# Performance work log

Measured on AMD Instinct MI355X. Metric: run time of the kernel, lower is better.

Reference implementation:

```python
import jax, jax.numpy as jnp
import numpy as np
import math

B, HW, E = 128, 3136, 96
NH, WS = 3, 7
EH = E // NH
NEG_INF = float('-inf')


def setup_inputs() -> dict:
    key = jax.random.key(0)
    ks = jax.random.split(key, 5)
    x = jax.random.normal(ks[0], (B, HW, E), dtype=jnp.float32)
    w1 = jax.random.normal(ks[1], (3 * E, E), dtype=jnp.float32) * 0.02
    b1 = jnp.zeros((3 * E,), dtype=jnp.float32)
    w2 = jax.random.normal(ks[2], (E, E), dtype=jnp.float32) * 0.02
    b2 = jnp.zeros((E,), dtype=jnp.float32)
    return {"x": x, "w1": w1, "b1": b1, "w2": w2, "b2": b2}


def _masks():
    m = WS * (WS // 2)  # 21
    row = jnp.zeros((WS * WS, WS * WS), dtype=jnp.float32)
    row = row.at[-m:, :-m].set(NEG_INF)
    row = row.at[:-m, -m:].set(NEG_INF)
    # rearrange '(r w1) (c w2) -> (w1 r) (w2 c)'
    col = row.reshape(WS, WS, WS, WS).transpose(1, 0, 3, 2).reshape(WS * WS, WS * WS)
    return row, col


def reference(x, w1, b1, w2, b2):
    b = x.shape[0]
    hh = ww = int(round(math.sqrt(x.shape[1])))
    nh, nw = hh // WS, ww // WS
    qkv = x @ w1.T + b1                      # [b, hw, 3E]
    qkv = qkv.reshape(b, hh, ww, E, 3)       # (c K) split, K=3
    # cyclic shift: (-WS)//2 == -4 (faithful to torch source)
    s = (-WS) // 2
    qkv = jnp.roll(qkv, (s, s), axis=(1, 2))
    # window partition: b (h m1) (w m2) (H E) K -> b H h w (m1 m2) E K
    t = qkv.reshape(b, nh, WS, nw, WS, NH, EH, 3)
    t = t.transpose(0, 5, 1, 3, 2, 4, 6, 7).reshape(b, NH, nh, nw, WS * WS, EH, 3)
    q, k, v = t[..., 0], t[..., 1], t[..., 2]
    att = jnp.einsum('bHxyqe,bHxyke->bHxyqk', q, k) / math.sqrt(EH)
    row_mask, col_mask = _masks()
    att = att.at[:, :, -1, :].add(row_mask)
    att = att.at[:, :, :, -1].add(col_mask)
    p = jax.nn.softmax(att, axis=-1)
    o = jnp.einsum('bHxyqk,bHxyke->bHxyqe', p, v)
    # reverse window partition: b H h w (m1 m2) E -> b (h m1) (w m2) (H E)
    o = o.reshape(b, NH, nh, nw, WS, WS, EH)
    o = o.transpose(0, 2, 4, 3, 5, 1, 6).reshape(b, hh, ww, E)
    o = jnp.roll(o, (WS // 2, WS // 2), axis=(1, 2))  # +3 (faithful)
    o = o.reshape(b, hh * ww, E)
    return o @ w2.T + b2
```

## Files before the change

### kernel.cpp

```cpp
#include <hip/hip_runtime.h>

typedef __attribute__((ext_vector_type(8))) __bf16 bf16x8;
typedef __attribute__((ext_vector_type(4))) float f32x4;
typedef __attribute__((ext_vector_type(4))) unsigned int u32x4;

__device__ __forceinline__ unsigned short f2bf(float f){
    unsigned int x = __builtin_bit_cast(unsigned int, f);
    x += 0x7FFFu + ((x >> 16) & 1u);
    return (unsigned short)(x >> 16);
}
__device__ __forceinline__ unsigned int pk2(float a, float b){
    return (unsigned int)f2bf(a) | ((unsigned int)f2bf(b) << 16);
}
__device__ __forceinline__ bf16x8 ldfrag(const unsigned short* p){
    u32x4 v = *reinterpret_cast<const u32x4*>(p);
    return __builtin_bit_cast(bf16x8, v);
}
__device__ __forceinline__ bf16x8 ldf32(const float* p){
    f32x4 a = *reinterpret_cast<const f32x4*>(p);
    f32x4 b = *reinterpret_cast<const f32x4*>(p + 4);
    u32x4 r;
    r[0] = pk2(a[0], a[1]); r[1] = pk2(a[2], a[3]);
    r[2] = pk2(b[0], b[1]); r[3] = pk2(b[2], b[3]);
    return __builtin_bit_cast(bf16x8, r);
}
__device__ __forceinline__ f32x4 mfma_bf16(bf16x8 a, bf16x8 b, f32x4 c){
    return __builtin_amdgcn_mfma_f32_16x16x32_bf16(a, b, c, 0, 0, 0);
}

#define W1F_SH 27648
#define W2F_SH 9216

__global__ __launch_bounds__(256) void k_prep(const float* __restrict__ w1,
                                              const float* __restrict__ b1,
                                              const float* __restrict__ w2,
                                              unsigned short* __restrict__ w1f,
                                              unsigned short* __restrict__ w2f,
                                              float* __restrict__ b1p)
{
    const float SCALE = 0.17677669529663687f;
    int i = blockIdx.x * 256 + threadIdx.x;
    if (i < 3456){
        int f = i >> 6, lane = i & 63;
        int n = f / 3, ks = f - n * 3;
        int l15 = lane & 15, qd = lane >> 4;
        int rp = n * 16 + l15;
        int c = rp / 96, rem = rp - c * 96;
        float s = (c == 0) ? SCALE : 1.0f;
        const float* src = w1 + (size_t)(3 * rem + c) * 96 + ks * 32 + qd * 8;
        f32x4 v0 = *reinterpret_cast<const f32x4*>(src);
        f32x4 v1 = *reinterpret_cast<const f32x4*>(src + 4);
        u32x4 p;
        p[0] = pk2(v0[0] * s, v0[1] * s); p[1] = pk2(v0[2] * s, v0[3] * s);
        p[2] = pk2(v1[0] * s, v1[1] * s); p[3] = pk2(v1[2] * s, v1[3] * s);
        *reinterpret_cast<u32x4*>(w1f + (size_t)f * 512 + lane * 8) = p;
    } else if (i < 4608){
        int j = i - 3456;
        int f = j >> 6, lane = j & 63;
        int n = f / 3, ks = f - n * 3;
        int l15 = lane & 15, qd = lane >> 4;
        const float* src = w2 + (size_t)(n * 16 + l15) * 96 + ks * 32 + qd * 8;
        f32x4 v0 = *reinterpret_cast<const f32x4*>(src);
        f32x4 v1 = *reinterpret_cast<const f32x4*>(src + 4);
        u32x4 p;
        p[0] = pk2(v0[0], v0[1]); p[1] = pk2(v0[2], v0[3]);
        p[2] = pk2(v1[0], v1[1]); p[3] = pk2(v1[2], v1[3]);
        *reinterpret_cast<u32x4*>(w2f + (size_t)f * 512 + lane * 8) = p;
    } else if (i < 4896){
        int rp = i - 4608;
        int c = rp / 96, rem = rp - c * 96;
        b1p[rp] = b1[3 * rem + c] * ((c == 0) ? SCALE : 1.0f);
    }
}

__global__ __launch_bounds__(256, 5) void k_fused(const float* __restrict__ x,
                                                  const unsigned short* __restrict__ w1f,
                                                  const float* __restrict__ b1p,
                                                  const unsigned short* __restrict__ w2f,
                                                  const float* __restrict__ b2,
                                                  float* __restrict__ out)
{
    __shared__ __align__(16) unsigned short smem[13056];
    unsigned short* Kr = smem;
    unsigned short* Vt = smem + 6144;
    float* o2 = reinterpret_cast<float*>(smem);

    const int tid = threadIdx.x;
    const int win = blockIdx.x;
    const int b = win >> 6, wy = (win >> 3) & 7, wx = win & 7;
    const int wave = tid >> 6, lane = tid & 63;
    const int l15 = lane & 15, qd = lane >> 4;
    const int s0 = (qd & 1) * 32 + l15;
    const int s1 = s0 + 16;

    bf16x8 bQf[3];
    {
        int pos = wave * 16 + l15;
        int iy = pos / 7, ix = pos - iy * 7;
        int h = wy * 7 + iy + 4; if (h >= 56) h -= 56;
        int w = wx * 7 + ix + 4; if (w >= 56) w -= 56;
        const float* xr = x + ((size_t)b * 3136 + h * 56 + w) * 96;
        bf16x8 aX0 = ldf32(xr + qd * 8);
        bf16x8 aX1 = ldf32(xr + 32 + qd * 8);
        bf16x8 aX2 = ldf32(xr + 64 + qd * 8);

        unsigned int Qw[12];
#pragma unroll
        for (int qt = 0; qt < 6; ++qt){
            const unsigned short* wf = w1f + (size_t)(qt * 3) * 512 + lane * 8;
            f32x4 a = {0.f, 0.f, 0.f, 0.f};
            a = mfma_bf16(ldfrag(wf),        aX0, a);
            a = mfma_bf16(ldfrag(wf + 512),  aX1, a);
            a = mfma_bf16(ldfrag(wf + 1024), aX2, a);
            f32x4 bq = *reinterpret_cast<const f32x4*>(b1p + qt * 16 + qd * 4);
            Qw[qt * 2]     = pk2(a[0] + bq[0], a[1] + bq[1]);
            Qw[qt * 2 + 1] = pk2(a[2] + bq[2], a[3] + bq[3]);
        }
#pragma unroll
        for (int H = 0; H < 3; ++H){
            u32x4 qw; unsigned int lo, hi;
            lo = (unsigned)__shfl((int)Qw[(2*H)*2],     s0, 64);
            hi = (unsigned)__shfl((int)Qw[(2*H+1)*2],   s0, 64); qw[0] = (qd & 2) ? hi : lo;
            lo = (unsigned)__shfl((int)Qw[(2*H)*2+1],   s0, 64);
            hi = (unsigned)__shfl((int)Qw[(2*H+1)*2+1], s0, 64); qw[1] = (qd & 2) ? hi : lo;
            lo = (unsigned)__shfl((int)Qw[(2*H)*2],     s1, 64);
            hi = (unsigned)__shfl((int)Qw[(2*H+1)*2],   s1, 64); qw[2] = (qd & 2) ? hi : lo;
            lo = (unsigned)__shfl((int)Qw[(2*H)*2+1],   s1, 64);
            hi = (unsigned)__shfl((int)Qw[(2*H+1)*2+1], s1, 64); qw[3] = (qd & 2) ? hi : lo;
            bQf[H] = __builtin_bit_cast(bf16x8, qw);
        }

#pragma unroll
        for (int n = 0; n < 6; ++n){
            const unsigned short* wf = w1f + (size_t)((6 + n) * 3) * 512 + lane * 8;
            f32x4 a = {0.f, 0.f, 0.f, 0.f};
            a = mfma_bf16(aX0, ldfrag(wf),        a);
            a = mfma_bf16(aX1, ldfrag(wf + 512),  a);
            a = mfma_bf16(aX2, ldfrag(wf + 1024), a);
            float bb = b1p[(6 + n) * 16 + l15];
            int H = n >> 1;
            int eh = ((n & 1) << 4) + l15;
            int ch = eh >> 3;
#pragma unroll
            for (int r = 0; r < 4; ++r){
                int p = wave * 16 + qd * 4 + r;
                int chs = ch ^ ((p >> 1) & 3);
                Kr[H * 2048 + p * 32 + chs * 8 + (eh & 7)] = f2bf(a[r] + bb);
            }
        }
#pragma unroll
        for (int n = 0; n < 6; ++n){
            const unsigned short* wf = w1f + (size_t)((12 + n) * 3) * 512 + lane * 8;
            f32x4 a = {0.f, 0.f, 0.f, 0.f};
            a = mfma_bf16(aX0, ldfrag(wf),        a);
            a = mfma_bf16(aX1, ldfrag(wf + 512),  a);
            a = mfma_bf16(aX2, ldfrag(wf + 1024), a);
            float bb = b1p[(12 + n) * 16 + l15];
            int H = n >> 1;
            int eh = ((n & 1) << 4) + l15;
#pragma unroll
            for (int r = 0; r < 4; ++r){
                int p = wave * 16 + qd * 4 + r;
                Vt[(H * 32 + eh) * 72 + p] = f2bf(a[r] + bb);
            }
        }
    }
    __syncthreads();

    const bool rowm = (wy == 7), colm = (wx == 7);
    const float NEGINF = -__builtin_inff();
    unsigned int m49 = 0, m28 = 0, m7 = 0;
#pragma unroll
    for (int tn = 0; tn < 4; ++tn)
#pragma unroll
        for (int r = 0; r < 4; ++r){
            int col = tn * 16 + qd * 4 + r;
            int bit = tn * 4 + r;
            m49 |= (unsigned)(col >= 49) << bit;
            m28 |= (unsigned)(col >= 28) << bit;
            m7  |= (unsigned)((col % 7) >= 4) << bit;
        }
    const int qrow = wave * 16 + l15;
    const bool rhi = (qrow >= 28);
    const bool rc7 = ((qrow % 7) >= 4);
    const int chq = qd ^ ((l15 >> 1) & 3);

    unsigned int Ow[12];
#pragma unroll
    for (int H = 0; H < 3; ++H){
        f32x4 S[4];
#pragma unroll
        for (int tn = 0; tn < 4; ++tn){
            bf16x8 aK = ldfrag(Kr + H * 2048 + (tn * 16 + l15) * 32 + chq * 8);
            f32x4 z = {0.f, 0.f, 0.f, 0.f};
            S[tn] = mfma_bf16(aK, bQf[H], z);
        }
        float mx = NEGINF;
#pragma unroll
        for (int tn = 0; tn < 4; ++tn)
#pragma unroll
            for (int r = 0; r < 4; ++r){
                int bit = tn * 4 + r;
                float v = S[tn][r];
                bool blocked = (((m49 >> bit) & 1u) != 0u)
                    || (rowm && (rhi != (((m28 >> bit) & 1u) != 0u)))
                    || (colm && (rc7 != (((m7 >> bit) & 1u) != 0u)));
                v = blocked ? NEGINF : v;
                S[tn][r] = v;
                mx = fmaxf(mx, v);
            }
        mx = fmaxf(mx, __shfl_xor(mx, 16, 64));
        mx = fmaxf(mx, __shfl_xor(mx, 32, 64));
        float sum = 0.f;
#pragma unroll
        for (int tn = 0; tn < 4; ++tn)
#pragma unroll
            for (int r = 0; r < 4; ++r){
                float e = exp2f((S[tn][r] - mx) * 1.4426950408889634f);
                S[tn][r] = e;
                sum += e;
            }
        sum += __shfl_xor(sum, 16, 64);
        sum += __shfl_xor(sum, 32, 64);
        float inv = 1.f / sum;

        unsigned int pkv[8];
#pragma unroll
        for (int tn = 0; tn < 4; ++tn){
            pkv[tn * 2]     = pk2(S[tn][0], S[tn][1]);
            pkv[tn * 2 + 1] = pk2(S[tn][2], S[tn][3]);
        }
        bf16x8 pF[2];
#pragma unroll
        for (int kt = 0; kt < 2; ++kt){
            u32x4 aw;
#pragma unroll
            for (int w4 = 0; w4 < 4; ++w4){
                int srcl = (w4 < 2) ? s0 : s1;
                unsigned int lo = (unsigned)__shfl((int)pkv[(2 * kt) * 2 + (w4 & 1)], srcl, 64);
                unsigned int hi = (unsigned)__shfl((int)pkv[(2 * kt + 1) * 2 + (w4 & 1)], srcl, 64);
                aw[w4] = (qd & 2) ? hi : lo;
            }
            pF[kt] = __builtin_bit_cast(bf16x8, aw);
        }
#pragma unroll
        for (int et = 0; et < 2; ++et){
            f32x4 o = {0.f, 0.f, 0.f, 0.f};
#pragma unroll
            for (int kt = 0; kt < 2; ++kt){
                bf16x8 aV = ldfrag(Vt + (H * 32 + et * 16 + l15) * 72 + kt * 32 + qd * 8);
                o = mfma_bf16(aV, pF[kt], o);
            }
            Ow[(H * 2 + et) * 2]     = pk2(o[0] * inv, o[1] * inv);
            Ow[(H * 2 + et) * 2 + 1] = pk2(o[2] * inv, o[3] * inv);
        }
    }

    bf16x8 aO[3];
#pragma unroll
    for (int c = 0; c < 3; ++c){
        u32x4 qw; unsigned int lo, hi;
        lo = (unsigned)__shfl((int)Ow[(2*c)*2],     s0, 64);
        hi = (unsigned)__shfl((int)Ow[(2*c+1)*2],   s0, 64); qw[0] = (qd & 2) ? hi : lo;
        lo = (unsigned)__shfl((int)Ow[(2*c)*2+1],   s0, 64);
        hi = (unsigned)__shfl((int)Ow[(2*c+1)*2+1], s0, 64); qw[1] = (qd & 2) ? hi : lo;
        lo = (unsigned)__shfl((int)Ow[(2*c)*2],     s1, 64);
        hi = (unsigned)__shfl((int)Ow[(2*c+1)*2],   s1, 64); qw[2] = (qd & 2) ? hi : lo;
        lo = (unsigned)__shfl((int)Ow[(2*c)*2+1],   s1, 64);
        hi = (unsigned)__shfl((int)Ow[(2*c+1)*2+1], s1, 64); qw[3] = (qd & 2) ? hi : lo;
        aO[c] = __builtin_bit_cast(bf16x8, qw);
    }

    f32x4 acc2[6];
#pragma unroll
    for (int n = 0; n < 6; ++n){
        const unsigned short* wf = w2f + (size_t)(n * 3) * 512 + lane * 8;
        f32x4 a = {0.f, 0.f, 0.f, 0.f};
        a = mfma_bf16(aO[0], ldfrag(wf),        a);
        a = mfma_bf16(aO[1], ldfrag(wf + 512),  a);
        a = mfma_bf16(aO[2], ldfrag(wf + 1024), a);
        acc2[n] = a;
    }
    __syncthreads();

#pragma unroll
    for (int n = 0; n < 6; ++n){
        float bb = b2[n * 16 + l15];
#pragma unroll
        for (int r = 0; r < 4; ++r)
            o2[(wave * 16 + qd * 4 + r) * 100 + n * 16 + l15] = acc2[n][r] + bb;
    }
    __syncthreads();

    {
        int row = tid >> 2, seg = tid & 3;
        if (row < 49){
            int iy = row / 7, ix = row - iy * 7;
            int h = wy * 7 + iy + 3; if (h >= 56) h -= 56;
            int w = wx * 7 + ix + 3; if (w >= 56) w -= 56;
            const float* src = o2 + row * 100 + seg * 24;
            float* dst = out + ((size_t)b * 3136 + h * 56 + w) * 96 + seg * 24;
#pragma unroll
            for (int v = 0; v < 6; ++v){
                f32x4 t4;
#pragma unroll
                for (int j = 0; j < 4; ++j) t4[j] = src[v * 4 + j];
                *reinterpret_cast<f32x4*>(dst + v * 4) = t4;
            }
        }
    }
}

extern "C" void kernel_launch(void* const* d_in, const int* in_sizes, int n_in,
                              void* d_out, int out_size, void* d_ws, size_t ws_size,
                              hipStream_t stream)
{
    const float* x  = (const float*)d_in[0];
    const float* w1 = (const float*)d_in[1];
    const float* b1 = (const float*)d_in[2];
    const float* w2 = (const float*)d_in[3];
    const float* b2 = (const float*)d_in[4];
    float* out = (float*)d_out;

    unsigned short* w1f = (unsigned short*)d_ws;
    unsigned short* w2f = w1f + W1F_SH;
    float* b1p = (float*)(w2f + W2F_SH);

    hipLaunchKernelGGL(k_prep,  dim3(20),   dim3(256), 0, stream, w1, b1, w2, w1f, w2f, b1p);
    hipLaunchKernelGGL(k_fused, dim3(8192), dim3(256), 0, stream, x, w1f, b1p, w2f, b2, out);
}
```

Measured before the change: 393.3 us.

## Use hardware bf16 pack, direct output stores, constant masks, higher occupancy

Replaces the software round-to-nearest bf16 conversion with the v_cvt_pk_bf16_f32 instruction throughout. V is now written to LDS as packed pairs, and the column mask bitfields are precomputed constants. The LDS staging of the output and its two barriers are removed; each lane writes its accumulator values straight to global memory in 64-byte row segments. Launch bounds are raised to request 6 blocks per CU. Together these cut ALU and synchronisation overhead, at the cost of less coalesced scalar output stores.

```diff
diff --git a/kernel.cpp b/kernel.cpp
--- a/kernel.cpp
+++ b/kernel.cpp
@@ -12,6 +12,14 @@
 __device__ __forceinline__ unsigned int pk2(float a, float b){
     return (unsigned int)f2bf(a) | ((unsigned int)f2bf(b) << 16);
 }
+__device__ __forceinline__ unsigned int cvtpk(float a, float b){
+    unsigned int r;
+    asm("v_cvt_pk_bf16_f32 %0, %1, %2" : "=v"(r) : "v"(a), "v"(b));
+    return r;
+}
+__device__ __forceinline__ unsigned short cvt1(float a){
+    return (unsigned short)(cvtpk(a, a) & 0xFFFFu);
+}
 __device__ __forceinline__ bf16x8 ldfrag(const unsigned short* p){
     u32x4 v = *reinterpret_cast<const u32x4*>(p);
     return __builtin_bit_cast(bf16x8, v);
@@ -20,8 +28,8 @@
     f32x4 a = *reinterpret_cast<const f32x4*>(p);
     f32x4 b = *reinterpret_cast<const f32x4*>(p + 4);
     u32x4 r;
-    r[0] = pk2(a[0], a[1]); r[1] = pk2(a[2], a[3]);
-    r[2] = pk2(b[0], b[1]); r[3] = pk2(b[2], b[3]);
+    r[0] = cvtpk(a[0], a[1]); r[1] = cvtpk(a[2], a[3]);
+    r[2] = cvtpk(b[0], b[1]); r[3] = cvtpk(b[2], b[3]);
     return __builtin_bit_cast(bf16x8, r);
 }
 __device__ __forceinline__ f32x4 mfma_bf16(bf16x8 a, bf16x8 b, f32x4 c){
@@ -73,7 +81,7 @@
     }
 }
 
-__global__ __launch_bounds__(256, 5) void k_fused(const float* __restrict__ x,
+__global__ __launch_bounds__(256, 6) void k_fused(const float* __restrict__ x,
                                                   const unsigned short* __restrict__ w1f,
                                                   const float* __restrict__ b1p,
                                                   const unsigned short* __restrict__ w2f,
@@ -83,7 +91,6 @@
     __shared__ __align__(16) unsigned short smem[13056];
     unsigned short* Kr = smem;
     unsigned short* Vt = smem + 6144;
-    float* o2 = reinterpret_cast<float*>(smem);
 
     const int tid = threadIdx.x;
     const int win = blockIdx.x;
@@ -113,8 +120,8 @@
             a = mfma_bf16(ldfrag(wf + 512),  aX1, a);
             a = mfma_bf16(ldfrag(wf + 1024), aX2, a);
             f32x4 bq = *reinterpret_cast<const f32x4*>(b1p + qt * 16 + qd * 4);
-            Qw[qt * 2]     = pk2(a[0] + bq[0], a[1] + bq[1]);
-            Qw[qt * 2 + 1] = pk2(a[2] + bq[2], a[3] + bq[3]);
+            Qw[qt * 2]     = cvtpk(a[0] + bq[0], a[1] + bq[1]);
+            Qw[qt * 2 + 1] = cvtpk(a[2] + bq[2], a[3] + bq[3]);
         }
 #pragma unroll
         for (int H = 0; H < 3; ++H){
@@ -145,7 +152,7 @@
             for (int r = 0; r < 4; ++r){
                 int p = wave * 16 + qd * 4 + r;
                 int chs = ch ^ ((p >> 1) & 3);
-                Kr[H * 2048 + p * 32 + chs * 8 + (eh & 7)] = f2bf(a[r] + bb);
+                Kr[H * 2048 + p * 32 + chs * 8 + (eh & 7)] = cvt1(a[r] + bb);
             }
         }
 #pragma unroll
@@ -158,28 +165,21 @@
             float bb = b1p[(12 + n) * 16 + l15];
             int H = n >> 1;
             int eh = ((n & 1) << 4) + l15;
-#pragma unroll
-            for (int r = 0; r < 4; ++r){
-                int p = wave * 16 + qd * 4 + r;
-                Vt[(H * 32 + eh) * 72 + p] = f2bf(a[r] + bb);
-            }
+            int p0 = wave * 16 + qd * 4;
+#pragma unroll
+            for (int rp = 0; rp < 2; ++rp)
+                *reinterpret_cast<unsigned int*>(&Vt[(H * 32 + eh) * 72 + p0 + 2 * rp])
+                    = cvtpk(a[2 * rp] + bb, a[2 * rp + 1] + bb);
         }
     }
     __syncthreads();
 
     const bool rowm = (wy == 7), colm = (wx == 7);
     const float NEGINF = -__builtin_inff();
-    unsigned int m49 = 0, m28 = 0, m7 = 0;
-#pragma unroll
-    for (int tn = 0; tn < 4; ++tn)
-#pragma unroll
-        for (int r = 0; r < 4; ++r){
-            int col = tn * 16 + qd * 4 + r;
-            int bit = tn * 4 + r;
-            m49 |= (unsigned)(col >= 49) << bit;
-            m28 |= (unsigned)(col >= 28) << bit;
-            m7  |= (unsigned)((col % 7) >= 4) << bit;
-        }
+    const unsigned int m49 = (qd == 0) ? 0xE000u : 0xF000u;
+    const unsigned int m28 = (qd == 3) ? 0xFFF0u : 0xFF00u;
+    const unsigned int m7  = (qd & 2) ? ((qd & 1) ? 0x7C03u : 0x03E8u)
+                                      : ((qd & 1) ? 0xE817u : 0x17C0u);
     const int qrow = wave * 16 + l15;
     const bool rhi = (qrow >= 28);
     const bool rc7 = ((qrow % 7) >= 4);
@@ -227,8 +227,8 @@
         unsigned int pkv[8];
 #pragma unroll
         for (int tn = 0; tn < 4; ++tn){
-            pkv[tn * 2]     = pk2(S[tn][0], S[tn][1]);
-            pkv[tn * 2 + 1] = pk2(S[tn][2], S[tn][3]);
+            pkv[tn * 2]     = cvtpk(S[tn][0], S[tn][1]);
+            pkv[tn * 2 + 1] = cvtpk(S[tn][2], S[tn][3]);
         }
         bf16x8 pF[2];
 #pragma unroll
@@ -251,8 +251,8 @@
                 bf16x8 aV = ldfrag(Vt + (H * 32 + et * 16 + l15) * 72 + kt * 32 + qd * 8);
                 o = mfma_bf16(aV, pF[kt], o);
             }
-            Ow[(H * 2 + et) * 2]     = pk2(o[0] * inv, o[1] * inv);
-            Ow[(H * 2 + et) * 2 + 1] = pk2(o[2] * inv, o[3] * inv);
+            Ow[(H * 2 + et) * 2]     = cvtpk(o[0] * inv, o[1] * inv);
+            Ow[(H * 2 + et) * 2 + 1] = cvtpk(o[2] * inv, o[3] * inv);
         }
     }
 
@@ -281,32 +281,21 @@
         a = mfma_bf16(aO[2], ldfrag(wf + 1024), a);
         acc2[n] = a;
     }
-    __syncthreads();
-
-#pragma unroll
-    for (int n = 0; n < 6; ++n){
-        float bb = b2[n * 16 + l15];
-#pragma unroll
-        for (int r = 0; r < 4; ++r)
-            o2[(wave * 16 + qd * 4 + r) * 100 + n * 16 + l15] = acc2[n][r] + bb;
-    }
-    __syncthreads();
-
-    {
-        int row = tid >> 2, seg = tid & 3;
+    float bb2[6];
+#pragma unroll
+    for (int n = 0; n < 6; ++n) bb2[n] = b2[n * 16 + l15];
+
+#pragma unroll
+    for (int r = 0; r < 4; ++r){
+        int row = wave * 16 + qd * 4 + r;
+        int iy = row / 7, ix = row - iy * 7;
+        int h = wy * 7 + iy + 3; if (h >= 56) h -= 56;
+        int w = wx * 7 + ix + 3; if (w >= 56) w -= 56;
+        float* dst = out + ((size_t)b * 3136 + h * 56 + w) * 96 + l15;
         if (row < 49){
-            int iy = row / 7, ix = row - iy * 7;
-            int h = wy * 7 + iy + 3; if (h >= 56) h -= 56;
-            int w = wx * 7 + ix + 3; if (w >= 56) w -= 56;
-            const float* src = o2 + row * 100 + seg * 24;
-            float* dst = out + ((size_t)b * 3136 + h * 56 + w) * 96 + seg * 24;
-#pragma unroll
-            for (int v = 0; v < 6; ++v){
-                f32x4 t4;
-#pragma unroll
-                for (int j = 0; j < 4; ++j) t4[j] = src[v * 4 + j];
-                *reinterpret_cast<f32x4*>(dst + v * 4) = t4;
-            }
+#pragma unroll
+            for (int n = 0; n < 6; ++n)
+                dst[n * 16] = acc2[n][r] + bb2[n];
         }
     }
 }
```

Measured after the change: 364.6 us. 7.3% less time.
